# Optimization experiments

Hardware: AMD Instinct MI355X
Metric: run time of the kernel (lower is better)

Reference implementation:

```python
import jax, jax.numpy as jnp
import numpy as np

NUM_HEADS = 12


def get_rel_pos(q_size, k_size, rel_pos):
    # rel_pos: (2*max(q,k)-1, C). Here q_size==k_size so no interpolation needed.
    q_coords = jnp.arange(q_size)[:, None] * max(k_size / q_size, 1.0)
    k_coords = jnp.arange(k_size)[None, :] * max(q_size / k_size, 1.0)
    rel = (q_coords - k_coords) + (k_size - 1) * max(q_size / k_size, 1.0)
    return rel_pos[rel.astype(jnp.int32)]  # (q_size, k_size, C)


def add_decomposed_rel_pos(attn, q, rel_pos_h, rel_pos_w, q_size, k_size):
    q_h, q_w = q_size
    k_h, k_w = k_size
    Rh = get_rel_pos(q_h, k_h, rel_pos_h)  # (q_h,k_h,C)
    Rw = get_rel_pos(q_w, k_w, rel_pos_w)  # (q_w,k_w,C)
    B, _, C = q.shape  # B = num_heads * batch
    r_q = q.reshape(B, q_h, q_w, C)
    rel_h = jnp.einsum('bhwc,hkc->bhwk', r_q, Rh)  # (B,q_h,q_w,k_h)
    rel_w = jnp.einsum('bhwc,wkc->bhwk', r_q, Rw)  # (B,q_h,q_w,k_w)
    attn = attn.reshape(B, q_h, q_w, k_h, k_w)
    attn = attn + rel_h[:, :, :, :, None] + rel_w[:, :, :, None, :]
    return attn.reshape(B, q_h * q_w, k_h * k_w)


def setup_inputs() -> dict:
    key = jax.random.key(0)
    ks = jax.random.split(key, 7)
    B, H, W, dim = 128, 14, 14, 768
    head_dim = dim // NUM_HEADS
    return {
        'x': jax.random.normal(ks[0], (B, H, W, dim), dtype=jnp.float32),
        'qkv_w': jax.random.normal(ks[1], (dim, 3 * dim), dtype=jnp.float32) * 0.02,
        'qkv_b': jax.random.normal(ks[2], (3 * dim,), dtype=jnp.float32) * 0.02,
        'proj_w': jax.random.normal(ks[3], (dim, dim), dtype=jnp.float32) * 0.02,
        'proj_b': jax.random.normal(ks[4], (dim,), dtype=jnp.float32) * 0.02,
        'rel_pos_h': jax.random.normal(ks[5], (2 * H - 1, head_dim), dtype=jnp.float32) * 0.02,
        'rel_pos_w': jax.random.normal(ks[6], (2 * W - 1, head_dim), dtype=jnp.float32) * 0.02,
    }


def reference(x, qkv_w, qkv_b, proj_w, proj_b, rel_pos_h, rel_pos_w):
    B, H, W, dim = x.shape
    nh = NUM_HEADS
    hd = dim // nh
    scale = hd ** -0.5
    L = H * W
    # qkv projection: (B,H,W,3*dim) -> (3, nh*B, L, hd)
    qkv = x.reshape(B, L, dim) @ qkv_w + qkv_b
    qkv = qkv.reshape(B, L, 3, nh, hd)
    qkv = jnp.transpose(qkv, (2, 3, 0, 1, 4)).reshape(3, nh * B, L, hd)
    q, k, v = qkv[0], qkv[1], qkv[2]
    attn = jnp.einsum('bqc,bkc->bqk', q * scale, k)  # (nh*B, L, L)
    attn = add_decomposed_rel_pos(attn, q, rel_pos_h, rel_pos_w, (H, W), (H, W))
    attn = jax.nn.softmax(attn, axis=-1)
    out = jnp.einsum('bqk,bkc->bqc', attn, v)  # (nh*B, L, hd)
    out = out.reshape(nh, B, H, W, hd)
    out = jnp.transpose(out, (1, 2, 3, 0, 4)).reshape(B, H, W, dim)
    return out @ proj_w + proj_b
```

## Files before the change

kernel.cpp:

```cpp
#include <hip/hip_runtime.h>
#include <stdint.h>

typedef unsigned short u16;
typedef __bf16 bf16x8 __attribute__((ext_vector_type(8)));
typedef u16 u16x8 __attribute__((ext_vector_type(8)));
typedef float f32x4 __attribute__((ext_vector_type(4)));

#define MFMA16(a,b,c) __builtin_amdgcn_mfma_f32_16x16x32_bf16((a),(b),(c),0,0,0)
#define GLOAD16(gp, lp) __builtin_amdgcn_global_load_lds( \
    (const __attribute__((address_space(1))) void*)(gp), \
    (__attribute__((address_space(3))) void*)(lp), 16, 0, 0)

__device__ __forceinline__ u16 f2bf(float f) {
  union { float f; uint32_t u; } v; v.f = f;
  return (u16)((v.u + 0x7FFFu + ((v.u >> 16) & 1u)) >> 16);
}
__device__ __forceinline__ float bits2f(uint32_t u) {
  union { uint32_t u; float f; } v; v.u = u; return v.f;
}
__device__ __forceinline__ uint32_t cvtpk(float lo, float hi) {
  uint32_t r;
  asm("v_cvt_pk_bf16_f32 %0, %1, %2" : "=v"(r) : "v"(lo), "v"(hi));
  return r;
}
__device__ __forceinline__ int4 pack8(const u16* v) {
  int4 r;
  r.x = (int)((uint32_t)v[0] | ((uint32_t)v[1] << 16));
  r.y = (int)((uint32_t)v[2] | ((uint32_t)v[3] << 16));
  r.z = (int)((uint32_t)v[4] | ((uint32_t)v[5] << 16));
  r.w = (int)((uint32_t)v[6] | ((uint32_t)v[7] << 16));
  return r;
}

__global__ void k_cvt(const float* __restrict__ in, u16* __restrict__ out, int n4) {
  int i = blockIdx.x * 256 + threadIdx.x;
  int stride = gridDim.x * 256;
  for (; i < n4; i += stride) {
    float4 v = reinterpret_cast<const float4*>(in)[i];
    ushort4 o;
    o.x = f2bf(v.x); o.y = f2bf(v.y); o.z = f2bf(v.z); o.w = f2bf(v.w);
    reinterpret_cast<ushort4*>(out)[i] = o;
  }
}

__global__ void k_transpose(const float* __restrict__ in, u16* __restrict__ out, int R, int C) {
  __shared__ float t[32][33];
  int tx = threadIdx.x & 31, ty = threadIdx.x >> 5;
  int c0 = blockIdx.x * 32, r0 = blockIdx.y * 32;
  #pragma unroll
  for (int i = 0; i < 4; i++)
    t[ty + i*8][tx] = in[(size_t)(r0 + ty + i*8) * C + (c0 + tx)];
  __syncthreads();
  #pragma unroll
  for (int i = 0; i < 4; i++)
    out[(size_t)(c0 + ty + i*8) * R + (r0 + tx)] = f2bf(t[tx][ty + i*8]);
}

__global__ __launch_bounds__(512, 2) void k_qkv256(
    const u16* __restrict__ A, const u16* __restrict__ BT, const float* __restrict__ bias,
    u16* __restrict__ qo, u16* __restrict__ ko, u16* __restrict__ vo)
{
  __shared__ u16 SMEM[65536];

  int bid0 = blockIdx.x;
  int xcd = bid0 & 7, idx = bid0 >> 3;
  int base = (xcd < 2) ? xcd * 111 : 2 * 111 + (xcd - 2) * 110;
  int wgid = base + idx;
  int mt = wgid / 9, nt = wgid - (wgid / 9) * 9;

  int tid = threadIdx.x, lane = tid & 63, w = tid >> 6;
  int g = lane >> 4, c4 = lane & 15;
  int wr = w >> 2, wc = w & 3;

  int c1 = tid, c2 = tid + 512;
  int pr1 = c1 >> 3, sl1 = (c1 & 7) ^ (pr1 & 7);
  int g1 = sl1 >> 1, row1 = pr1 * 2 + (sl1 & 1);
  int pr2 = c2 >> 3, sl2 = (c2 & 7) ^ (pr2 & 7);
  int g2 = sl2 >> 1, row2 = pr2 * 2 + (sl2 & 1);

  const u16* pA1 = A + (size_t)(mt * 256 + row1) * 768 + g1 * 8;
  const u16* pA2 = A + (size_t)(mt * 256 + row2) * 768 + g2 * 8;
  const u16* pB1 = BT + (size_t)(nt * 256 + row1) * 768 + g1 * 8;
  const u16* pB2 = BT + (size_t)(nt * 256 + row2) * 768 + g2 * 8;

  int prc = c4 >> 1;
  int slotRd = (2 * g + (c4 & 1)) ^ prc;
  int aoff = wr * 4096 + prc * 64 + slotRd * 8;
  int boff = wc * 2048 + prc * 64 + slotRd * 8;

  f32x4 acc[8][4];
  f32x4 z4 = {0.f, 0.f, 0.f, 0.f};
  #pragma unroll
  for (int f = 0; f < 8; f++)
    #pragma unroll
    for (int fc = 0; fc < 4; fc++) acc[f][fc] = z4;

  #pragma unroll
  for (int kk = 0; kk < 3; kk++) {
    u16* dA = SMEM + (kk << 13);
    GLOAD16(pA1 + kk * 32, dA + c1 * 8);
    GLOAD16(pA2 + kk * 32, dA + c2 * 8);
    u16* dB = SMEM + 32768 + (kk << 13);
    GLOAD16(pB1 + kk * 32, dB + c1 * 8);
    GLOAD16(pB2 + kk * 32, dB + c2 * 8);
  }
  asm volatile("s_waitcnt vmcnt(8)" ::: "memory");
  __builtin_amdgcn_s_barrier();

  for (int k = 0; k < 24; ++k) {
    const u16* As = SMEM + ((k & 3) << 13);
    const u16* Bs = SMEM + 32768 + ((k & 3) << 13);
    bf16x8 bfr[4], afr[4];
    #pragma unroll
    for (int fc = 0; fc < 4; fc++) bfr[fc] = *(const bf16x8*)(Bs + boff + fc * 512);
    #pragma unroll
    for (int f = 0; f < 4; f++) afr[f] = *(const bf16x8*)(As + aoff + f * 512);
    if (k < 21) {
      u16* d = SMEM + (((k + 3) & 3) << 13);
      GLOAD16(pA1 + (k + 3) * 32, d + c1 * 8);
      GLOAD16(pA2 + (k + 3) * 32, d + c2 * 8);
      asm volatile("s_waitcnt vmcnt(6)" ::: "memory");
    } else if (k == 21) {
      asm volatile("s_waitcnt vmcnt(0)" ::: "memory");
    }
    __builtin_amdgcn_s_barrier();
    #pragma unroll
    for (int f = 0; f < 4; f++)
      #pragma unroll
      for (int fc = 0; fc < 4; fc++)
        acc[f][fc] = MFMA16(afr[f], bfr[fc], acc[f][fc]);

    #pragma unroll
    for (int f = 0; f < 4; f++) afr[f] = *(const bf16x8*)(As + aoff + (4 + f) * 512);
    if (k < 21) {
      u16* d = SMEM + 32768 + (((k + 3) & 3) << 13);
      GLOAD16(pB1 + (k + 3) * 32, d + c1 * 8);
      GLOAD16(pB2 + (k + 3) * 32, d + c2 * 8);
      asm volatile("s_waitcnt vmcnt(6)" ::: "memory");
    }
    __builtin_amdgcn_s_barrier();
    #pragma unroll
    for (int f = 0; f < 4; f++)
      #pragma unroll
      for (int fc = 0; fc < 4; fc++)
        acc[4 + f][fc] = MFMA16(afr[f], bfr[fc], acc[4 + f][fc]);
  }

  __builtin_amdgcn_s_barrier();
  u16* Ob = SMEM + w * 8192;

  int i3 = nt / 3;
  u16* dst = (i3 == 0) ? qo : (i3 == 1) ? ko : vo;
  int head = (nt - i3 * 3) * 4 + wc;
  float bsv[4];
  #pragma unroll
  for (int fc = 0; fc < 4; fc++) bsv[fc] = bias[nt * 256 + wc * 64 + fc * 16 + c4];

  #pragma unroll
  for (int f = 0; f < 8; f++)
    #pragma unroll
    for (int fc = 0; fc < 4; fc++)
      #pragma unroll
      for (int j = 0; j < 4; j++)
        Ob[(f * 16 + 4 * g + j) * 64 + fc * 16 + c4] = f2bf(acc[f][fc][j] + bsv[fc]);

  int m0 = mt * 256 + wr * 128;
  #pragma unroll
  for (int it2 = 0; it2 < 16; ++it2) {
    int cc = it2 * 64 + lane;
    int row = cc >> 3, kc = cc & 7;
    int mm = m0 + row;
    int bb2 = mm / 196, ll = mm - bb2 * 196;
    int4 v = *(const int4*)(Ob + row * 64 + kc * 8);
    *(int4*)(dst + ((size_t)((head * 128 + bb2) * 196 + ll)) * 64 + kc * 8) = v;
  }
}

template<int KDIM>
__device__ __forceinline__ void gemm_core(
    const u16* __restrict__ A, const u16* __restrict__ BT,
    int mt, int nt, f32x4 acc[4][4], u16* As, u16* Bs)
{
  int tid = threadIdx.x, lane = tid & 63, w = tid >> 6;
  int g = lane >> 4, c4 = lane & 15;
  int wr = w >> 1, wc = w & 1;
  int srow = lane >> 2;
  int pslot = (lane & 3) ^ ((lane >> 3) & 3);
  int rsel = g ^ ((c4 >> 1) & 3);
  const size_t abase = (size_t)(mt * 128) * KDIM;
  const size_t bbase = (size_t)(nt * 128) * KDIM;
  for (int kt = 0; kt < KDIM / 32; kt++) {
    __syncthreads();
    #pragma unroll
    for (int cc = 0; cc < 2; cc++) {
      int cid = w * 2 + cc;
      int row = cid * 16 + srow;
      GLOAD16(A + abase + (size_t)row * KDIM + kt * 32 + pslot * 8, As + cid * 512);
      GLOAD16(BT + bbase + (size_t)row * KDIM + kt * 32 + pslot * 8, Bs + cid * 512);
    }
    __syncthreads();
    bf16x8 af[4], bfv[4];
    #pragma unroll
    for (int f = 0; f < 4; f++) {
      af[f]  = *(const bf16x8*)(As + (wr * 64 + f * 16 + c4) * 32 + rsel * 8);
      bfv[f] = *(const bf16x8*)(Bs + (wc * 64 + f * 16 + c4) * 32 + rsel * 8);
    }
    #pragma unroll
    for (int fr = 0; fr < 4; fr++)
      #pragma unroll
      for (int fc = 0; fc < 4; fc++)
        acc[fr][fc] = MFMA16(af[fr], bfv[fc], acc[fr][fc]);
  }
}

__global__ __launch_bounds__(256, 3) void k_proj_gemm(
    const u16* __restrict__ A, const u16* __restrict__ BT, const float* __restrict__ bias,
    float* __restrict__ out)
{
  __shared__ u16 As[128 * 32], Bs[128 * 32];
  int bid0 = blockIdx.x;
  int bid = (bid0 & 7) * 147 + (bid0 >> 3);
  int nt = bid % 6, mt = bid / 6;
  f32x4 z = {0.f, 0.f, 0.f, 0.f};
  f32x4 acc[4][4];
  #pragma unroll
  for (int i = 0; i < 4; i++)
    #pragma unroll
    for (int j = 0; j < 4; j++) acc[i][j] = z;
  gemm_core<768>(A, BT, mt, nt, acc, As, Bs);

  int tid = threadIdx.x, lane = tid & 63, w = tid >> 6;
  int g = lane >> 4, c4 = lane & 15;
  int wr = w >> 1, wc = w & 1;
  #pragma unroll
  for (int fc = 0; fc < 4; fc++) {
    int n0 = nt * 128 + wc * 64 + fc * 16 + c4;
    float bs = bias[n0];
    #pragma unroll
    for (int fr = 0; fr < 4; fr++)
      #pragma unroll
      for (int j = 0; j < 4; j++) {
        int m = mt * 128 + wr * 64 + fr * 16 + g * 4 + j;
        out[(size_t)m * 768 + n0] = acc[fr][fc][j] + bs;
      }
  }
}

#define VP 216
__global__ __launch_bounds__(256, 2) void k_attn(
    const u16* __restrict__ Q, const u16* __restrict__ Kg, const u16* __restrict__ Vg,
    const u16* __restrict__ RPH, const u16* __restrict__ RPW, u16* __restrict__ Ows)
{
  __shared__ u16 K64[208 * 64];
  __shared__ u16 Krel[208 * 40];
  __shared__ u16 VT[64 * VP];
  __shared__ u16 QO[4][1024];

  int bh = blockIdx.x;
  int hh = bh >> 7, bb = bh & 127;
  int tid = threadIdx.x, lane = tid & 63, w = tid >> 6;
  int g = lane >> 4, c4 = lane & 15;

  const u16* kbase = Kg + (size_t)bh * 12544;
  const u16* vbase = Vg + (size_t)bh * 12544;
  const u16* qbase = Q + (size_t)bh * 12544;

  for (int ch = tid; ch < 1664; ch += 256) {
    int row = ch >> 3, s = ch & 7;
    u16 outv[8];
    if (row < 196) {
      u16x8 v = *(const u16x8*)(kbase + row * 64 + s * 8);
      #pragma unroll
      for (int e = 0; e < 8; e++)
        outv[e] = f2bf(bits2f((uint32_t)v[e] << 16) * 0.125f);
    } else {
      #pragma unroll
      for (int e = 0; e < 8; e++) outv[e] = 0;
    }
    *(int4*)(K64 + row * 64 + ((s ^ (row & 7)) * 8)) = pack8(outv);
  }
  if (tid < 208) {
    int k = tid;
    int kh = k / 14, kw2 = k - kh * 14;
    #pragma unroll
    for (int s = 0; s < 5; s++) {
      u16 vals[8];
      #pragma unroll
      for (int e = 0; e < 8; e++) {
        int c = s * 8 + e;
        u16 x = 0;
        if (k < 196) {
          if (c == kh) x = 0x3F80;
          else if (c == 14 + kw2) x = 0x3F80;
        } else {
          if (c == 28) x = 0x3F80;
        }
        vals[e] = x;
      }
      *(int4*)(Krel + k * 40 + s * 8) = pack8(vals);
    }
  }
  for (int i = tid; i < 64 * 20; i += 256) {
    int chn = i / 20, col = 196 + (i - chn * 20);
    VT[chn * VP + col] = 0;
  }
  for (int ch2 = tid; ch2 < 784; ch2 += 256) {
    int kp = ch2 >> 3, cb = ch2 & 7;
    int key = kp * 2, cz = cb * 8;
    u16x8 a = *(const u16x8*)(vbase + key * 64 + cz);
    u16x8 b2 = *(const u16x8*)(vbase + (key + 1) * 64 + cz);
    int kk = key & 31;
    int colp = (key >> 5) * 32 + ((kk & 15) >> 2) * 8 + (kk & 3) + ((kk >> 4) << 2);
    #pragma unroll
    for (int j = 0; j < 8; j++) {
      uint32_t pk = (uint32_t)a[j] | ((uint32_t)b2[j] << 16);
      *(uint32_t*)(VT + (cz + j) * VP + colp) = pk;
    }
  }
  __syncthreads();

  int t1 = 16 + c4; if (t1 > 26) t1 = 26;
  bf16x8 rh00 = *(const bf16x8*)(RPH + c4 * 64 + g * 8);
  bf16x8 rh01 = *(const bf16x8*)(RPH + c4 * 64 + 32 + g * 8);
  bf16x8 rh10 = *(const bf16x8*)(RPH + t1 * 64 + g * 8);
  bf16x8 rh11 = *(const bf16x8*)(RPH + t1 * 64 + 32 + g * 8);
  bf16x8 rw00 = *(const bf16x8*)(RPW + c4 * 64 + g * 8);
  bf16x8 rw01 = *(const bf16x8*)(RPW + c4 * 64 + 32 + g * 8);
  bf16x8 rw10 = *(const bf16x8*)(RPW + t1 * 64 + g * 8);
  bf16x8 rw11 = *(const bf16x8*)(RPW + t1 * 64 + 32 + g * 8);

  f32x4 z4 = {0.f, 0.f, 0.f, 0.f};
  int sw = c4 & 7;

  for (int qt = w; qt < 13; qt += 4) {
    int qi = qt * 16 + c4;
    int qrow = qi > 195 ? 195 : qi;
    bf16x8 qa0 = *(const bf16x8*)(qbase + qrow * 64 + g * 8);
    bf16x8 qa1 = *(const bf16x8*)(qbase + qrow * 64 + 32 + g * 8);

    u16* Qr = (u16*)QO[w];
    {
      int4 zz = {0, 0, 0, 0};
      int zr = lane >> 2, zs = lane & 3;
      *(int4*)(Qr + zr * 64 + ((zs ^ (zr & 7)) * 8)) = zz;
    }
    if (g == 0) Qr[c4 * 64 + (28 ^ (sw << 3))] = f2bf(-30000.f);

    int qh = qi / 14;
    int qwv = qi - qh * 14;

    f32x4 e0 = MFMA16(rh00, qa0, z4); e0 = MFMA16(rh01, qa1, e0);
    f32x4 e1 = MFMA16(rh10, qa0, z4); e1 = MFMA16(rh11, qa1, e1);
    #pragma unroll
    for (int tt = 0; tt < 2; tt++) {
      f32x4 e = tt ? e1 : e0;
      #pragma unroll
      for (int j = 0; j < 4; j++) {
        int t = tt * 16 + 4 * g + j;
        int kh = qh + 13 - t;
        if ((unsigned)kh <= 13u) Qr[c4 * 64 + (kh ^ (sw << 3))] = f2bf(e[j]);
      }
    }
    f32x4 f0 = MFMA16(rw00, qa0, z4); f0 = MFMA16(rw01, qa1, f0);
    f32x4 f1 = MFMA16(rw10, qa0, z4); f1 = MFMA16(rw11, qa1, f1);
    #pragma unroll
    for (int tt = 0; tt < 2; tt++) {
      f32x4 e = tt ? f1 : f0;
      #pragma unroll
      for (int j = 0; j < 4; j++) {
        int t = tt * 16 + 4 * g + j;
        int kw3 = qwv + 13 - t;
        if ((unsigned)kw3 <= 13u) Qr[c4 * 64 + ((14 + kw3) ^ (sw << 3))] = f2bf(e[j]);
      }
    }

    bf16x8 qrelB = *(const bf16x8*)(Qr + c4 * 64 + ((g ^ sw) * 8));

    f32x4 St[13];
    #pragma unroll
    for (int i = 0; i < 13; i++) {
      int key = i * 16 + c4;
      const u16* kr = K64 + key * 64;
      int swk = key & 7;
      bf16x8 kb0 = *(const bf16x8*)(kr + ((g ^ swk) * 8));
      bf16x8 kb1 = *(const bf16x8*)(kr + (((4 + g) ^ swk) * 8));
      f32x4 acc = MFMA16(kb0, qa0, z4);
      acc = MFMA16(kb1, qa1, acc);
      bf16x8 krl = *(const bf16x8*)(Krel + key * 40 + g * 8);
      St[i] = MFMA16(krl, qrelB, acc);
    }

    float mx = -3.0e38f;
    #pragma unroll
    for (int i = 0; i < 13; i++)
      #pragma unroll
      for (int j = 0; j < 4; j++) mx = fmaxf(mx, St[i][j]);
    mx = fmaxf(mx, __shfl_xor(mx, 16));
    mx = fmaxf(mx, __shfl_xor(mx, 32));

    float ls = 0.f;
    f32x4 O[4] = {z4, z4, z4, z4};
    #pragma unroll
    for (int p = 0; p < 7; p++) {
      float pe[8];
      #pragma unroll
      for (int j2 = 0; j2 < 4; j2++) { pe[j2] = __expf(St[2 * p][j2] - mx); ls += pe[j2]; }
      if (p < 6) {
        #pragma unroll
        for (int j2 = 0; j2 < 4; j2++) { pe[4 + j2] = __expf(St[2 * p + 1][j2] - mx); ls += pe[4 + j2]; }
      } else {
        #pragma unroll
        for (int j2 = 0; j2 < 4; j2++) pe[4 + j2] = 0.f;
      }
      union { uint32_t u[4]; bf16x8 v; } pb;
      pb.u[0] = cvtpk(pe[0], pe[1]);
      pb.u[1] = cvtpk(pe[2], pe[3]);
      pb.u[2] = cvtpk(pe[4], pe[5]);
      pb.u[3] = cvtpk(pe[6], pe[7]);
      #pragma unroll
      for (int ct = 0; ct < 4; ct++) {
        bf16x8 va = *(const bf16x8*)(VT + (ct * 16 + c4) * VP + p * 32 + g * 8);
        O[ct] = MFMA16(va, pb.v, O[ct]);
      }
    }
    ls += __shfl_xor(ls, 16);
    ls += __shfl_xor(ls, 32);

    float inv = 1.f / ls;
    #pragma unroll
    for (int ct = 0; ct < 4; ct++) {
      uint32_t o0 = cvtpk(O[ct][0] * inv, O[ct][1] * inv);
      uint32_t o1 = cvtpk(O[ct][2] * inv, O[ct][3] * inv);
      uint2 ov = {o0, o1};
      *(uint2*)(Qr + c4 * 64 + ((ct * 16 + g * 4) ^ (sw << 3))) = ov;
    }
    #pragma unroll
    for (int it = 0; it < 2; ++it) {
      int cc = it * 64 + lane;
      int row = cc >> 3, kc = cc & 7;
      int q = qt * 16 + row;
      if (q < 196) {
        int4 v = *(const int4*)(Qr + row * 64 + ((kc ^ (row & 7)) * 8));
        *(int4*)(Ows + (size_t)(bb * 196 + q) * 768 + hh * 64 + kc * 8) = v;
      }
    }
  }
}

extern "C" void kernel_launch(void* const* d_in, const int* in_sizes, int n_in,
                              void* d_out, int out_size, void* d_ws, size_t ws_size,
                              hipStream_t stream) {
  (void)in_sizes; (void)n_in; (void)out_size; (void)ws_size;
  const float* x      = (const float*)d_in[0];
  const float* qkv_w  = (const float*)d_in[1];
  const float* qkv_b  = (const float*)d_in[2];
  const float* proj_w = (const float*)d_in[3];
  const float* proj_b = (const float*)d_in[4];
  const float* rph    = (const float*)d_in[5];
  const float* rpw    = (const float*)d_in[6];
  float* out = (float*)d_out;
  char* ws = (char*)d_ws;

  u16* xb   = (u16*)(ws);
  u16* wT   = (u16*)(ws + 38535168);
  u16* pT   = (u16*)(ws + 42074112);
  u16* rphb = (u16*)(ws + 43253760);
  u16* rpwb = (u16*)(ws + 43257856);
  u16* qws  = (u16*)(ws + 43261952);
  u16* kws  = (u16*)(ws + 81797120);
  u16* vws  = (u16*)(ws + 120332288);
  u16* Ows  = xb;

  k_cvt<<<2048, 256, 0, stream>>>(x, xb, 4816896);
  k_cvt<<<2, 256, 0, stream>>>(rph, rphb, 432);
  k_cvt<<<2, 256, 0, stream>>>(rpw, rpwb, 432);
  k_transpose<<<dim3(72, 24), 256, 0, stream>>>(qkv_w, wT, 768, 2304);
  k_transpose<<<dim3(24, 24), 256, 0, stream>>>(proj_w, pT, 768, 768);
  k_qkv256<<<882, 512, 0, stream>>>(xb, wT, qkv_b, qws, kws, vws);
  k_attn<<<1536, 256, 0, stream>>>(qws, kws, vws, rphb, rpwb, Ows);
  k_proj_gemm<<<196 * 6, 256, 0, stream>>>(Ows, pT, proj_b, out);
}
```

Measured before the change: 275.2 us.

## Pipeline proj GEMM with multi-stage async loads and streamline epilogues

Replaces the single-buffered proj GEMM with a 4-stage ring of direct-to-LDS async loads and swizzled LDS reads, mirroring the QKV kernel's pipeline. It also adds s_setprio around the MFMA blocks in both GEMMs. The QKV and attention epilogues now write global memory directly from registers instead of staging through LDS. The attention kernel shrinks its per-wave Q-rel buffer and changes the VT padding. The direct epilogue stores are narrower and less coalesced, so they risk more memory transactions in exchange for fewer LDS round trips.

Measured after the change: 261.7 us. -4.9%, faster.

```diff
diff --git a/kernel.cpp b/kernel.cpp
--- a/kernel.cpp
+++ b/kernel.cpp
@@ -124,11 +124,13 @@
       asm volatile("s_waitcnt vmcnt(0)" ::: "memory");
     }
     __builtin_amdgcn_s_barrier();
+    __builtin_amdgcn_s_setprio(1);
     #pragma unroll
     for (int f = 0; f < 4; f++)
       #pragma unroll
       for (int fc = 0; fc < 4; fc++)
         acc[f][fc] = MFMA16(afr[f], bfr[fc], acc[f][fc]);
+    __builtin_amdgcn_s_setprio(0);
 
     #pragma unroll
     for (int f = 0; f < 4; f++) afr[f] = *(const bf16x8*)(As + aoff + (4 + f) * 512);
@@ -139,15 +141,14 @@
       asm volatile("s_waitcnt vmcnt(6)" ::: "memory");
     }
     __builtin_amdgcn_s_barrier();
+    __builtin_amdgcn_s_setprio(1);
     #pragma unroll
     for (int f = 0; f < 4; f++)
       #pragma unroll
       for (int fc = 0; fc < 4; fc++)
         acc[4 + f][fc] = MFMA16(afr[f], bfr[fc], acc[4 + f][fc]);
-  }
-
-  __builtin_amdgcn_s_barrier();
-  u16* Ob = SMEM + w * 8192;
+    __builtin_amdgcn_s_setprio(0);
+  }
 
   int i3 = nt / 3;
   u16* dst = (i3 == 0) ? qo : (i3 == 1) ? ko : vo;
@@ -156,82 +157,102 @@
   #pragma unroll
   for (int fc = 0; fc < 4; fc++) bsv[fc] = bias[nt * 256 + wc * 64 + fc * 16 + c4];
 
-  #pragma unroll
-  for (int f = 0; f < 8; f++)
-    #pragma unroll
-    for (int fc = 0; fc < 4; fc++)
-      #pragma unroll
-      for (int j = 0; j < 4; j++)
-        Ob[(f * 16 + 4 * g + j) * 64 + fc * 16 + c4] = f2bf(acc[f][fc][j] + bsv[fc]);
-
-  int m0 = mt * 256 + wr * 128;
-  #pragma unroll
-  for (int it2 = 0; it2 < 16; ++it2) {
-    int cc = it2 * 64 + lane;
-    int row = cc >> 3, kc = cc & 7;
-    int mm = m0 + row;
-    int bb2 = mm / 196, ll = mm - bb2 * 196;
-    int4 v = *(const int4*)(Ob + row * 64 + kc * 8);
-    *(int4*)(dst + ((size_t)((head * 128 + bb2) * 196 + ll)) * 64 + kc * 8) = v;
-  }
-}
-
-template<int KDIM>
-__device__ __forceinline__ void gemm_core(
-    const u16* __restrict__ A, const u16* __restrict__ BT,
-    int mt, int nt, f32x4 acc[4][4], u16* As, u16* Bs)
+  int mbase = mt * 256 + wr * 128 + g * 4;
+  #pragma unroll
+  for (int f = 0; f < 8; f++) {
+    #pragma unroll
+    for (int j = 0; j < 4; j++) {
+      int mm = mbase + f * 16 + j;
+      int bb2 = mm / 196, ll = mm - bb2 * 196;
+      size_t ro = (size_t)((head * 128 + bb2) * 196 + ll) * 64;
+      #pragma unroll
+      for (int fc = 0; fc < 4; fc++)
+        dst[ro + fc * 16 + c4] = f2bf(acc[f][fc][j] + bsv[fc]);
+    }
+  }
+}
+
+__global__ __launch_bounds__(256, 2) void k_proj256(
+    const u16* __restrict__ A, const u16* __restrict__ BT, const float* __restrict__ bias,
+    float* __restrict__ out)
 {
+  __shared__ u16 SMEM[32768];
+
+  int bid0 = blockIdx.x;
+  int bid = (bid0 & 7) * 147 + (bid0 >> 3);
+  int nt = bid % 6, mt = bid / 6;
+
   int tid = threadIdx.x, lane = tid & 63, w = tid >> 6;
   int g = lane >> 4, c4 = lane & 15;
   int wr = w >> 1, wc = w & 1;
-  int srow = lane >> 2;
-  int pslot = (lane & 3) ^ ((lane >> 3) & 3);
-  int rsel = g ^ ((c4 >> 1) & 3);
-  const size_t abase = (size_t)(mt * 128) * KDIM;
-  const size_t bbase = (size_t)(nt * 128) * KDIM;
-  for (int kt = 0; kt < KDIM / 32; kt++) {
-    __syncthreads();
-    #pragma unroll
-    for (int cc = 0; cc < 2; cc++) {
-      int cid = w * 2 + cc;
-      int row = cid * 16 + srow;
-      GLOAD16(A + abase + (size_t)row * KDIM + kt * 32 + pslot * 8, As + cid * 512);
-      GLOAD16(BT + bbase + (size_t)row * KDIM + kt * 32 + pslot * 8, Bs + cid * 512);
-    }
-    __syncthreads();
-    bf16x8 af[4], bfv[4];
-    #pragma unroll
-    for (int f = 0; f < 4; f++) {
-      af[f]  = *(const bf16x8*)(As + (wr * 64 + f * 16 + c4) * 32 + rsel * 8);
-      bfv[f] = *(const bf16x8*)(Bs + (wc * 64 + f * 16 + c4) * 32 + rsel * 8);
-    }
-    #pragma unroll
-    for (int fr = 0; fr < 4; fr++)
+
+  int c1 = tid, c2 = tid + 256;
+  int pr1 = c1 >> 3, sl1 = (c1 & 7) ^ (pr1 & 7);
+  int g1 = sl1 >> 1, row1 = pr1 * 2 + (sl1 & 1);
+  int pr2 = c2 >> 3, sl2 = (c2 & 7) ^ (pr2 & 7);
+  int g2 = sl2 >> 1, row2 = pr2 * 2 + (sl2 & 1);
+
+  const u16* pA1 = A + (size_t)(mt * 128 + row1) * 768 + g1 * 8;
+  const u16* pA2 = A + (size_t)(mt * 128 + row2) * 768 + g2 * 8;
+  const u16* pB1 = BT + (size_t)(nt * 128 + row1) * 768 + g1 * 8;
+  const u16* pB2 = BT + (size_t)(nt * 128 + row2) * 768 + g2 * 8;
+
+  int prc = c4 >> 1;
+  int slotRd = (2 * g + (c4 & 1)) ^ prc;
+  int aoff = wr * 2048 + prc * 64 + slotRd * 8;
+  int boff = wc * 2048 + prc * 64 + slotRd * 8;
+
+  f32x4 acc[4][4];
+  f32x4 z4 = {0.f, 0.f, 0.f, 0.f};
+  #pragma unroll
+  for (int f = 0; f < 4; f++)
+    #pragma unroll
+    for (int fc = 0; fc < 4; fc++) acc[f][fc] = z4;
+
+  #pragma unroll
+  for (int kk = 0; kk < 3; kk++) {
+    u16* dA = SMEM + (kk << 12);
+    GLOAD16(pA1 + kk * 32, dA + c1 * 8);
+    GLOAD16(pA2 + kk * 32, dA + c2 * 8);
+    u16* dB = SMEM + 16384 + (kk << 12);
+    GLOAD16(pB1 + kk * 32, dB + c1 * 8);
+    GLOAD16(pB2 + kk * 32, dB + c2 * 8);
+  }
+  asm volatile("s_waitcnt vmcnt(8)" ::: "memory");
+  __builtin_amdgcn_s_barrier();
+
+  for (int k = 0; k < 24; ++k) {
+    const u16* As = SMEM + ((k & 3) << 12);
+    const u16* Bs = SMEM + 16384 + ((k & 3) << 12);
+    bf16x8 bfr[4], afr[4];
+    #pragma unroll
+    for (int fc = 0; fc < 4; fc++) bfr[fc] = *(const bf16x8*)(Bs + boff + fc * 512);
+    #pragma unroll
+    for (int f = 0; f < 4; f++) afr[f] = *(const bf16x8*)(As + aoff + f * 512);
+    if (k < 21) {
+      u16* dA = SMEM + (((k + 3) & 3) << 12);
+      GLOAD16(pA1 + (k + 3) * 32, dA + c1 * 8);
+      GLOAD16(pA2 + (k + 3) * 32, dA + c2 * 8);
+      u16* dB = SMEM + 16384 + (((k + 3) & 3) << 12);
+      GLOAD16(pB1 + (k + 3) * 32, dB + c1 * 8);
+      GLOAD16(pB2 + (k + 3) * 32, dB + c2 * 8);
+      asm volatile("s_waitcnt vmcnt(8)" ::: "memory");
+    } else if (k == 21) {
+      asm volatile("s_waitcnt vmcnt(4)" ::: "memory");
+    } else if (k == 22) {
+      asm volatile("s_waitcnt vmcnt(0)" ::: "memory");
+    }
+    __builtin_amdgcn_s_barrier();
+    __builtin_amdgcn_s_setprio(1);
+    #pragma unroll
+    for (int f = 0; f < 4; f++)
       #pragma unroll
       for (int fc = 0; fc < 4; fc++)
-        acc[fr][fc] = MFMA16(af[fr], bfv[fc], acc[fr][fc]);
-  }
-}
-
-__global__ __launch_bounds__(256, 3) void k_proj_gemm(
-    const u16* __restrict__ A, const u16* __restrict__ BT, const float* __restrict__ bias,
-    float* __restrict__ out)
-{
-  __shared__ u16 As[128 * 32], Bs[128 * 32];
-  int bid0 = blockIdx.x;
-  int bid = (bid0 & 7) * 147 + (bid0 >> 3);
-  int nt = bid % 6, mt = bid / 6;
-  f32x4 z = {0.f, 0.f, 0.f, 0.f};
-  f32x4 acc[4][4];
-  #pragma unroll
-  for (int i = 0; i < 4; i++)
-    #pragma unroll
-    for (int j = 0; j < 4; j++) acc[i][j] = z;
-  gemm_core<768>(A, BT, mt, nt, acc, As, Bs);
-
-  int tid = threadIdx.x, lane = tid & 63, w = tid >> 6;
-  int g = lane >> 4, c4 = lane & 15;
-  int wr = w >> 1, wc = w & 1;
+        acc[f][fc] = MFMA16(afr[f], bfr[fc], acc[f][fc]);
+    __builtin_amdgcn_s_setprio(0);
+    __builtin_amdgcn_s_barrier();
+  }
+
   #pragma unroll
   for (int fc = 0; fc < 4; fc++) {
     int n0 = nt * 128 + wc * 64 + fc * 16 + c4;
@@ -246,7 +267,7 @@
   }
 }
 
-#define VP 216
+#define VP 232
 __global__ __launch_bounds__(256, 2) void k_attn(
     const u16* __restrict__ Q, const u16* __restrict__ Kg, const u16* __restrict__ Vg,
     const u16* __restrict__ RPH, const u16* __restrict__ RPW, u16* __restrict__ Ows)
@@ -254,7 +275,7 @@
   __shared__ u16 K64[208 * 64];
   __shared__ u16 Krel[208 * 40];
   __shared__ u16 VT[64 * VP];
-  __shared__ u16 QO[4][1024];
+  __shared__ u16 Qrel[4][16 * 40];
 
   int bh = blockIdx.x;
   int hh = bh >> 7, bb = bh & 127;
@@ -300,9 +321,9 @@
       *(int4*)(Krel + k * 40 + s * 8) = pack8(vals);
     }
   }
-  for (int i = tid; i < 64 * 20; i += 256) {
-    int chn = i / 20, col = 196 + (i - chn * 20);
-    VT[chn * VP + col] = 0;
+  for (int i = tid; i < 2048; i += 256) {
+    int chn = i >> 5, c = 192 + (i & 31);
+    if (c >= 196 && c < VP) VT[chn * VP + c] = 0;
   }
   for (int ch2 = tid; ch2 < 784; ch2 += 256) {
     int kp = ch2 >> 3, cb = ch2 & 7;
@@ -330,7 +351,6 @@
   bf16x8 rw11 = *(const bf16x8*)(RPW + t1 * 64 + 32 + g * 8);
 
   f32x4 z4 = {0.f, 0.f, 0.f, 0.f};
-  int sw = c4 & 7;
 
   for (int qt = w; qt < 13; qt += 4) {
     int qi = qt * 16 + c4;
@@ -338,13 +358,13 @@
     bf16x8 qa0 = *(const bf16x8*)(qbase + qrow * 64 + g * 8);
     bf16x8 qa1 = *(const bf16x8*)(qbase + qrow * 64 + 32 + g * 8);
 
-    u16* Qr = (u16*)QO[w];
+    u16* Qr = (u16*)Qrel[w];
     {
       int4 zz = {0, 0, 0, 0};
-      int zr = lane >> 2, zs = lane & 3;
-      *(int4*)(Qr + zr * 64 + ((zs ^ (zr & 7)) * 8)) = zz;
-    }
-    if (g == 0) Qr[c4 * 64 + (28 ^ (sw << 3))] = f2bf(-30000.f);
+      *(int4*)(Qr + lane * 8) = zz;
+      if (lane < 16) *(int4*)(Qr + 512 + lane * 8) = zz;
+      if (g == 0) Qr[c4 * 40 + 28] = f2bf(-30000.f);
+    }
 
     int qh = qi / 14;
     int qwv = qi - qh * 14;
@@ -358,7 +378,7 @@
       for (int j = 0; j < 4; j++) {
         int t = tt * 16 + 4 * g + j;
         int kh = qh + 13 - t;
-        if ((unsigned)kh <= 13u) Qr[c4 * 64 + (kh ^ (sw << 3))] = f2bf(e[j]);
+        if ((unsigned)kh <= 13u) Qr[c4 * 40 + kh] = f2bf(e[j]);
       }
     }
     f32x4 f0 = MFMA16(rw00, qa0, z4); f0 = MFMA16(rw01, qa1, f0);
@@ -370,20 +390,20 @@
       for (int j = 0; j < 4; j++) {
         int t = tt * 16 + 4 * g + j;
         int kw3 = qwv + 13 - t;
-        if ((unsigned)kw3 <= 13u) Qr[c4 * 64 + ((14 + kw3) ^ (sw << 3))] = f2bf(e[j]);
-      }
-    }
-
-    bf16x8 qrelB = *(const bf16x8*)(Qr + c4 * 64 + ((g ^ sw) * 8));
+        if ((unsigned)kw3 <= 13u) Qr[c4 * 40 + 14 + kw3] = f2bf(e[j]);
+      }
+    }
+
+    bf16x8 qrelB = *(const bf16x8*)(Qr + c4 * 40 + g * 8);
 
     f32x4 St[13];
     #pragma unroll
     for (int i = 0; i < 13; i++) {
       int key = i * 16 + c4;
       const u16* kr = K64 + key * 64;
-      int swk = key & 7;
-      bf16x8 kb0 = *(const bf16x8*)(kr + ((g ^ swk) * 8));
-      bf16x8 kb1 = *(const bf16x8*)(kr + (((4 + g) ^ swk) * 8));
+      int sw = key & 7;
+      bf16x8 kb0 = *(const bf16x8*)(kr + ((g ^ sw) * 8));
+      bf16x8 kb1 = *(const bf16x8*)(kr + (((4 + g) ^ sw) * 8));
       f32x4 acc = MFMA16(kb0, qa0, z4);
       acc = MFMA16(kb1, qa1, acc);
       bf16x8 krl = *(const bf16x8*)(Krel + key * 40 + g * 8);
@@ -426,22 +446,15 @@
     ls += __shfl_xor(ls, 16);
     ls += __shfl_xor(ls, 32);
 
-    float inv = 1.f / ls;
-    #pragma unroll
-    for (int ct = 0; ct < 4; ct++) {
-      uint32_t o0 = cvtpk(O[ct][0] * inv, O[ct][1] * inv);
-      uint32_t o1 = cvtpk(O[ct][2] * inv, O[ct][3] * inv);
-      uint2 ov = {o0, o1};
-      *(uint2*)(Qr + c4 * 64 + ((ct * 16 + g * 4) ^ (sw << 3))) = ov;
-    }
-    #pragma unroll
-    for (int it = 0; it < 2; ++it) {
-      int cc = it * 64 + lane;
-      int row = cc >> 3, kc = cc & 7;
-      int q = qt * 16 + row;
-      if (q < 196) {
-        int4 v = *(const int4*)(Qr + row * 64 + ((kc ^ (row & 7)) * 8));
-        *(int4*)(Ows + (size_t)(bb * 196 + q) * 768 + hh * 64 + kc * 8) = v;
+    if (qi < 196) {
+      float inv = 1.f / ls;
+      size_t obase = (size_t)(bb * 196 + qi) * 768 + hh * 64;
+      #pragma unroll
+      for (int ct = 0; ct < 4; ct++) {
+        uint32_t o0 = cvtpk(O[ct][0] * inv, O[ct][1] * inv);
+        uint32_t o1 = cvtpk(O[ct][2] * inv, O[ct][3] * inv);
+        uint2 ov = {o0, o1};
+        *(uint2*)(Ows + obase + ct * 16 + g * 4) = ov;
       }
     }
   }
@@ -478,5 +491,5 @@
   k_transpose<<<dim3(24, 24), 256, 0, stream>>>(proj_w, pT, 768, 768);
   k_qkv256<<<882, 512, 0, stream>>>(xb, wT, qkv_b, qws, kws, vws);
   k_attn<<<1536, 256, 0, stream>>>(qws, kws, vws, rphb, rpwb, Ows);
-  k_proj_gemm<<<196 * 6, 256, 0, stream>>>(Ows, pT, proj_b, out);
-}
+  k_proj256<<<1176, 256, 0, stream>>>(Ows, pT, proj_b, out);
+}
```
